# Kernel optimization log

Measured on AMD Instinct MI355X. Metric: run time of the kernel, lower is better.

The kernel has to match this reference:

```python
import jax, jax.numpy as jnp
import numpy as np

B, S, F, H = 64, 1024, 64, 128


def setup_inputs() -> dict:
    key = jax.random.key(0)
    ks = jax.random.split(key, 12)
    s = 1.0 / np.sqrt(H)
    u = lambda k, shape: jax.random.uniform(k, shape, jnp.float32, -s, s)
    return {
        "x": jax.random.normal(ks[0], (B, S, F), jnp.float32),
        "mu": jax.random.normal(ks[1], (B, 1, F), jnp.float32),
        "W_ih0": u(ks[2], (4 * H, F)),
        "W_hh0": u(ks[3], (4 * H, H)),
        "b_ih0": u(ks[4], (4 * H,)),
        "b_hh0": u(ks[5], (4 * H,)),
        "W_ih1": u(ks[6], (4 * H, H)),
        "W_hh1": u(ks[7], (4 * H, H)),
        "b_ih1": u(ks[8], (4 * H,)),
        "b_hh1": u(ks[9], (4 * H,)),
        "fc_w": u(ks[10], (1, H)),
        "fc_b": u(ks[11], (1,)),
    }


def _cell(x_gates, h, c, Whh, bias):
    # PyTorch LSTM cell: gates ordered i, f, g, o
    g = x_gates + h @ Whh.T + bias
    i, f, gg, o = jnp.split(g, 4, axis=-1)
    c = jax.nn.sigmoid(f) * c + jax.nn.sigmoid(i) * jnp.tanh(gg)
    h = jax.nn.sigmoid(o) * jnp.tanh(c)
    return h, c


def _lstm2(x1, x2, Wih, Whh, bih, bhh):
    # 2-step LSTM layer from zero initial state; returns per-step hidden states
    bias = bih + bhh
    n = x1.shape[0]
    hd = Whh.shape[1]
    h0 = jnp.zeros((n, hd), x1.dtype)
    h1, c1 = _cell(x1 @ Wih.T, h0, h0, Whh, bias)
    h2, _ = _cell(x2 @ Wih.T, h1, c1, Whh, bias)
    return h1, h2


def reference(x, mu, W_ih0, W_hh0, b_ih0, b_hh0, W_ih1, W_hh1, b_ih1, b_hh1, fc_w, fc_b):
    b, s, f = x.shape
    # Every timestep runs an independent 2-step LSTM [x_t, mu] from zero state,
    # so fold (batch, seq) into one big batch of B*S instances.
    x1 = x.reshape(b * s, f)                                   # step-1 inputs
    x2 = jnp.broadcast_to(mu, (b, s, f)).reshape(b * s, f)     # step-2 inputs (mu)
    h1, h2 = _lstm2(x1, x2, W_ih0, W_hh0, b_ih0, b_hh0)        # layer 0
    _, h2 = _lstm2(h1, h2, W_ih1, W_hh1, b_ih1, b_hh1)         # layer 1
    h = jax.nn.relu(h2).reshape(b, s, -1)                      # relu; dropout is identity (eval)
    out = h @ fc_w.T + fc_b                                    # [B, S, 1]
    return out
```

## Files before the change

### kernel.cpp

```cpp
#include <hip/hip_runtime.h>


typedef _Float16 half8 __attribute__((ext_vector_type(8)));
typedef _Float16 half4_t __attribute__((ext_vector_type(4)));
typedef float f32x4 __attribute__((ext_vector_type(4)));

#define L2E  1.4426950408889634f
#define L2E2 2.8853900817779268f

#define WP_WIH0 0
#define WP_WHH0 32768
#define WP_WIH1 98304
#define WP_WHH1 163840
#define WS_BIAS0 458752
#define WS_BIAS1 (458752 + 2048)
#define WS_MUG2  (458752 + 4096)

__global__ void prep_kernel(const float* __restrict__ Wih0,
                            const float* __restrict__ Whh0,
                            const float* __restrict__ Wih1,
                            const float* __restrict__ Whh1,
                            const float* __restrict__ bih0,
                            const float* __restrict__ bhh0,
                            const float* __restrict__ bih1,
                            const float* __restrict__ bhh1,
                            const float* __restrict__ mu,
                            _Float16* __restrict__ Wp,
                            float* __restrict__ bias0f,
                            float* __restrict__ bias1f,
                            float* __restrict__ mu_g2)
{
    int blk = blockIdx.x;
    if (blk >= 113) {
        int o = (blk - 113) * 256 + threadIdx.x;
        int b = o >> 9;
        int n = o & 511;
        float s = bih0[n] + bhh0[n];
        const float* m = mu + b * 64;
        const float* wrow = Wih0 + n * 64;
        #pragma unroll 8
        for (int k = 0; k < 64; ++k) s += m[k] * wrow[k];
        float scale = ((n >> 7) == 2) ? L2E2 : L2E;
        mu_g2[o] = s * scale;
        return;
    }
    if (blk == 112) {
        int i = threadIdx.x;
        float sc_hi = (i < 128) ? L2E2 : L2E;
        bias0f[i]       = (bih0[i]       + bhh0[i])       * L2E;
        bias0f[i + 256] = (bih0[i + 256] + bhh0[i + 256]) * sc_hi;
        bias1f[i]       = (bih1[i]       + bhh1[i])       * L2E;
        bias1f[i + 256] = (bih1[i + 256] + bhh1[i + 256]) * sc_hi;
        return;
    }
    int gidx = blk * 256 + threadIdx.x;
    const float* src; int KC, Kw, local;
    if (gidx < 4096)       { src = Wih0; KC = 2; Kw = 64;  local = gidx; }
    else if (gidx < 12288) { src = Whh0; KC = 4; Kw = 128; local = gidx - 4096; }
    else if (gidx < 20480) { src = Wih1; KC = 4; Kw = 128; local = gidx - 12288; }
    else                   { src = Whh1; KC = 4; Kw = 128; local = gidx - 20480; }
    int lane = local & 63;
    int tmp  = local >> 6;
    int kc   = tmp % KC;
    int nt   = tmp / KC;
    int n  = nt * 16 + (lane & 15);
    int k0 = kc * 32 + (lane >> 4) * 8;
    float scale = ((n >> 7) == 2) ? L2E2 : L2E;
    const float* s = src + n * Kw + k0;
    half8 hv;
    #pragma unroll
    for (int j = 0; j < 8; ++j) hv[j] = (_Float16)(s[j] * scale);
    *(half8*)(Wp + (size_t)gidx * 8) = hv;
}

__device__ __forceinline__ float sig2(float a) {
    return __builtin_amdgcn_rcpf(1.0f + __builtin_amdgcn_exp2f(-a));
}
__device__ __forceinline__ float sigtanh(float xs, float yt) {
    float d = __builtin_amdgcn_exp2f(-xs);
    float e = __builtin_amdgcn_exp2f(yt);
    return (e - 1.0f) * __builtin_amdgcn_rcpf((1.0f + d) * (1.0f + e));
}

__device__ __forceinline__ int swz(int row, int col) {
    return (row << 8) + (col ^ ((row & 7) << 4));
}

__device__ __forceinline__ void lds_barrier() {
    asm volatile("s_waitcnt lgkmcnt(0)" ::: "memory");
    __builtin_amdgcn_s_barrier();
    asm volatile("" ::: "memory");
}

template<bool SKIPF>
__device__ __forceinline__ void load_bq(half8 bq[4], const _Float16* __restrict__ Wq,
                                        int KC, int kc, int w, int lane)
{
    #pragma unroll
    for (int g = 0; g < 4; ++g) {
        if (SKIPF && g == 1) continue;
        bq[g] = *(const half8*)(Wq + (((g * 8 + w) * KC + kc) * 64 + lane) * 8);
    }
}

template<int SRC>
__device__ __forceinline__ void load_a(half8 a[4], const char* base, int kc, int c, int q)
{
    #pragma unroll
    for (int mt = 0; mt < 4; ++mt) {
        if (SRC == 0)
            a[mt] = *(const half8*)((const _Float16*)base + (mt * 16 + c) * 72 + kc * 32 + q * 8);
        else
            a[mt] = *(const half8*)(base + swz(mt * 16 + c, kc * 64 + q * 16));
    }
}

template<int KC, int SRC, bool PF, bool FIRST, bool SKIPF, bool NSKIPF>
__device__ __forceinline__ void gemm_pf(const _Float16* __restrict__ Wq,
                                        const char* Abase,
                                        const _Float16* __restrict__ Wnext, int KCnext,
                                        half8 bqc[4], const f32x4 bv[4],
                                        int w, int lane, f32x4 acc[4][4])
{
    const int c = lane & 15, q = lane >> 4;
    #pragma unroll
    for (int kc = 0; kc < KC; ++kc) {
        half8 bqn[4];
        if (kc + 1 < KC)  load_bq<SKIPF>(bqn, Wq, KC, kc + 1, w, lane);
        else if (PF)      load_bq<NSKIPF>(bqn, Wnext, KCnext, 0, w, lane);
        half8 a[4];
        load_a<SRC>(a, Abase, kc, c, q);
        __builtin_amdgcn_s_setprio(1);
        #pragma unroll
        for (int mt = 0; mt < 4; ++mt)
            #pragma unroll
            for (int g = 0; g < 4; ++g) {
                if (SKIPF && g == 1) continue;
                f32x4 cin = (FIRST && kc == 0) ? bv[g] : acc[mt][g];
                acc[mt][g] = __builtin_amdgcn_mfma_f32_16x16x32_f16(bqc[g], a[mt], cin, 0, 0, 0);
            }
        __builtin_amdgcn_s_setprio(0);
        if (kc + 1 < KC) {
            #pragma unroll
            for (int g = 0; g < 4; ++g)
                if (!(SKIPF && g == 1)) bqc[g] = bqn[g];
        } else if (PF) {
            #pragma unroll
            for (int g = 0; g < 4; ++g)
                if (!(NSKIPF && g == 1)) bqc[g] = bqn[g];
        }
    }
}

__global__ __launch_bounds__(512) void lstm_main(
    const float* __restrict__ x, const _Float16* __restrict__ Wp_in,
    const float* __restrict__ bias0f_in, const float* __restrict__ bias1f_in,
    const float* __restrict__ mu_g2_in, const float* __restrict__ fc_w_in,
    const float* __restrict__ fc_b_in, float* __restrict__ out)
{
    __shared__ __align__(16) char smem[49152];
    char* H1s  = smem;
    char* H2s  = smem + 16384;
    char* H11s = smem + 32768;
    _Float16* A0 = (_Float16*)(smem + 16384);

    const int t = threadIdx.x;
    const int w = t >> 6, lane = t & 63, c = lane & 15, q = lane >> 4;
    const int wg = blockIdx.x;
    const int b = wg >> 4;
    const int bq_idx = w * 4 + q;

    half8 bqc[4];
    load_bq<true>(bqc, Wp_in + WP_WIH0, 2, 0, w, lane);

    {
        const float* xp = x + (size_t)wg * 4096 + t * 8;
        float4 u0 = ((const float4*)xp)[0];
        float4 u1 = ((const float4*)xp)[1];
        half8 hv;
        hv[0] = (_Float16)u0.x; hv[1] = (_Float16)u0.y;
        hv[2] = (_Float16)u0.z; hv[3] = (_Float16)u0.w;
        hv[4] = (_Float16)u1.x; hv[5] = (_Float16)u1.y;
        hv[6] = (_Float16)u1.z; hv[7] = (_Float16)u1.w;
        *(half8*)(A0 + (t >> 3) * 72 + (t & 7) * 8) = hv;
        if (t < 64) out[(size_t)wg * 64 + t] = fc_b_in[0];
    }
    lds_barrier();

    f32x4 acc[4][4];
    float cc[4][4];

    {
        f32x4 bv[4];
        {
            const float* bias0f = bias0f_in; asm volatile("" : "+s"(bias0f));
            #pragma unroll
            for (int g = 0; g < 4; ++g)
                if (g != 1) bv[g] = ((const f32x4*)bias0f)[g * 32 + bq_idx];
        }
        gemm_pf<2, 0, true, true, true, false>(
            Wp_in + WP_WIH0, (const char*)A0,
            Wp_in + WP_WHH0, 4, bqc, bv, w, lane, acc);
    }
    #pragma unroll
    for (int mt = 0; mt < 4; ++mt) {
        half4_t hv;
        #pragma unroll
        for (int r = 0; r < 4; ++r) {
            float c1 = sigtanh(acc[mt][0][r], acc[mt][2][r]);
            cc[mt][r] = c1;
            hv[r] = (_Float16)sigtanh(acc[mt][3][r], c1 * L2E2);
        }
        *(half4_t*)(H1s + swz(mt * 16 + c, w * 32 + q * 8)) = hv;
    }
    lds_barrier();

    {
        f32x4 bv[4];
        {
            const float* mu_g2b = mu_g2_in + b * 512; asm volatile("" : "+s"(mu_g2b));
            #pragma unroll
            for (int g = 0; g < 4; ++g)
                bv[g] = ((const f32x4*)mu_g2b)[g * 32 + bq_idx];
        }
        gemm_pf<4, 1, true, true, false, true>(
            Wp_in + WP_WHH0, H1s,
            Wp_in + WP_WIH1, 4, bqc, bv, w, lane, acc);
    }
    #pragma unroll
    for (int mt = 0; mt < 4; ++mt) {
        half4_t hv;
        #pragma unroll
        for (int r = 0; r < 4; ++r) {
            float c2 = sig2(acc[mt][1][r]) * cc[mt][r]
                     + sigtanh(acc[mt][0][r], acc[mt][2][r]);
            hv[r] = (_Float16)sigtanh(acc[mt][3][r], c2 * L2E2);
        }
        *(half4_t*)(H2s + swz(mt * 16 + c, w * 32 + q * 8)) = hv;
    }

    {
        f32x4 bv[4];
        {
            const float* bias1f = bias1f_in; asm volatile("" : "+s"(bias1f));
            #pragma unroll
            for (int g = 0; g < 4; ++g)
                if (g != 1) bv[g] = ((const f32x4*)bias1f)[g * 32 + bq_idx];
        }
        gemm_pf<4, 1, true, true, true, false>(
            Wp_in + WP_WIH1, H1s,
            Wp_in + WP_WIH1, 4, bqc, bv, w, lane, acc);
    }
    #pragma unroll
    for (int mt = 0; mt < 4; ++mt) {
        half4_t hv;
        #pragma unroll
        for (int r = 0; r < 4; ++r) {
            float c1 = sigtanh(acc[mt][0][r], acc[mt][2][r]);
            cc[mt][r] = c1;
            hv[r] = (_Float16)sigtanh(acc[mt][3][r], c1 * L2E2);
        }
        *(half4_t*)(H11s + swz(mt * 16 + c, w * 32 + q * 8)) = hv;
    }
    lds_barrier();

    {
        f32x4 bv[4];
        {
            const float* bias1f = bias1f_in; asm volatile("" : "+s"(bias1f));
            #pragma unroll
            for (int g = 0; g < 4; ++g)
                bv[g] = ((const f32x4*)bias1f)[g * 32 + bq_idx];
        }
        gemm_pf<4, 1, true, true, false, false>(
            Wp_in + WP_WIH1, H2s,
            Wp_in + WP_WHH1, 4, bqc, bv, w, lane, acc);
    }
    gemm_pf<4, 1, false, false, false, false>(
        Wp_in + WP_WHH1, H11s,
        nullptr, 0, bqc, nullptr, w, lane, acc);

    {
        const float* fc_w = fc_w_in; asm volatile("" : "+s"(fc_w));
        f32x4 fwv = ((const f32x4*)fc_w)[bq_idx];
        #pragma unroll
        for (int mt = 0; mt < 4; ++mt) {
            float v = 0.0f;
            #pragma unroll
            for (int r = 0; r < 4; ++r) {
                float c2 = sig2(acc[mt][1][r]) * cc[mt][r]
                         + sigtanh(acc[mt][0][r], acc[mt][2][r]);
                float h  = sigtanh(acc[mt][3][r], c2 * L2E2);
                v = fmaf(fmaxf(h, 0.0f), fwv[r], v);
            }
            v += __shfl_xor(v, 16);
            v += __shfl_xor(v, 32);
            if (lane < 16)
                atomicAdd(out + (size_t)wg * 64 + mt * 16 + lane, v);
        }
    }
}

extern "C" void kernel_launch(void* const* d_in, const int* in_sizes, int n_in,
                              void* d_out, int out_size, void* d_ws, size_t ws_size,
                              hipStream_t stream)
{
    const float* x    = (const float*)d_in[0];
    const float* mu   = (const float*)d_in[1];
    const float* Wih0 = (const float*)d_in[2];
    const float* Whh0 = (const float*)d_in[3];
    const float* bih0 = (const float*)d_in[4];
    const float* bhh0 = (const float*)d_in[5];
    const float* Wih1 = (const float*)d_in[6];
    const float* Whh1 = (const float*)d_in[7];
    const float* bih1 = (const float*)d_in[8];
    const float* bhh1 = (const float*)d_in[9];
    const float* fcw  = (const float*)d_in[10];
    const float* fcb  = (const float*)d_in[11];
    float* out = (float*)d_out;

    _Float16* Wp  = (_Float16*)d_ws;
    float* bias0f = (float*)((char*)d_ws + WS_BIAS0);
    float* bias1f = (float*)((char*)d_ws + WS_BIAS1);
    float* mu_g2  = (float*)((char*)d_ws + WS_MUG2);

    hipLaunchKernelGGL(prep_kernel, dim3(241), dim3(256), 0, stream,
                       Wih0, Whh0, Wih1, Whh1, bih0, bhh0, bih1, bhh1, mu,
                       Wp, bias0f, bias1f, mu_g2);
    hipLaunchKernelGGL(lstm_main, dim3(1024), dim3(512), 0, stream,
                       x, Wp, bias0f, bias1f, mu_g2, fcw, fcb, out);
}
```

Baseline: 132.4 us.

## Double-buffer weight fragment loads with inline-asm global loads and explicit vmcnt waits

Replaces the single-register weight prefetch with two ping-pong register buffers filled by inline-asm global_load_dwordx4 using immediate offsets and a scalar base. Explicit s_waitcnt vmcnt(4) waits let two k-chunks of weights stay in flight, and bias vectors for the next stage are issued early instead of reloaded just before each GEMM. The goal is to hide global-load latency behind MFMA work across stage boundaries. In exchange it takes on fragile manual vmcnt accounting, since the waits must match the order in which loads were issued, and more register pressure.

```diff
diff --git a/kernel.cpp b/kernel.cpp
--- a/kernel.cpp
+++ b/kernel.cpp
@@ -92,64 +92,87 @@
     asm volatile("" ::: "memory");
 }
 
-template<bool SKIPF>
-__device__ __forceinline__ void load_bq(half8 bq[4], const _Float16* __restrict__ Wq,
-                                        int KC, int kc, int w, int lane)
+template<int OFF>
+__device__ __forceinline__ void gload(half8 &d, unsigned vo, const _Float16* sbase) {
+    asm volatile("global_load_dwordx4 %0, %1, %2 offset:%c3"
+                 : "=v"(d) : "v"(vo), "s"(sbase), "n"(OFF));
+}
+template<int OFF>
+__device__ __forceinline__ void gloadf(f32x4 &d, unsigned vo, const float* sbase) {
+    asm volatile("global_load_dwordx4 %0, %1, %2 offset:%c3"
+                 : "=v"(d) : "v"(vo), "s"(sbase), "n"(OFF));
+}
+#define WAIT4(s) \
+    asm volatile("s_waitcnt vmcnt(4)" : "+v"((s)[0]), "+v"((s)[1]), "+v"((s)[2]), "+v"((s)[3]))
+#define WAIT4B(s, b) \
+    asm volatile("s_waitcnt vmcnt(4)" : "+v"((s)[0]), "+v"((s)[1]), "+v"((s)[2]), "+v"((s)[3]), \
+                                        "+v"((b)[0]), "+v"((b)[1]), "+v"((b)[2]), "+v"((b)[3]))
+#define WAIT0(s) \
+    asm volatile("s_waitcnt vmcnt(0)" : "+v"((s)[0]), "+v"((s)[1]), "+v"((s)[2]), "+v"((s)[3]))
+
+template<int OFF>
+__device__ __forceinline__ void issue4(half8 s[4], const unsigned vo[4],
+                                       const _Float16* base) {
+    gload<OFF>(s[0], vo[0], base);
+    gload<OFF>(s[1], vo[1], base);
+    gload<OFF>(s[2], vo[2], base);
+    gload<OFF>(s[3], vo[3], base);
+}
+__device__ __forceinline__ void issue_bias(f32x4 bv[4], unsigned vof, const float* base) {
+    gloadf<0>   (bv[0], vof, base);
+    gloadf<512> (bv[1], vof, base);
+    gloadf<1024>(bv[2], vof, base);
+    gloadf<1536>(bv[3], vof, base);
+}
+
+__device__ __forceinline__ void load_a0(half8 a[4], const _Float16* A0,
+                                        int kc, int c, int q) {
+    #pragma unroll
+    for (int mt = 0; mt < 4; ++mt)
+        a[mt] = *(const half8*)(A0 + (mt * 16 + c) * 72 + kc * 32 + q * 8);
+}
+__device__ __forceinline__ void load_aH(half8 a[4], const char* Hb,
+                                        int kc, int c, int q) {
+    #pragma unroll
+    for (int mt = 0; mt < 4; ++mt)
+        a[mt] = *(const half8*)(Hb + swz(mt * 16 + c, kc * 64 + q * 16));
+}
+
+template<bool SKIPF, bool CIN_BV>
+__device__ __forceinline__ void mm(const half8 s[4], const half8 a[4],
+                                   const f32x4 bv[4], f32x4 acc[4][4]) {
+    __builtin_amdgcn_s_setprio(1);
+    #pragma unroll
+    for (int mt = 0; mt < 4; ++mt)
+        #pragma unroll
+        for (int g = 0; g < 4; ++g) {
+            if (SKIPF && g == 1) continue;
+            f32x4 cin = CIN_BV ? bv[g] : acc[mt][g];
+            acc[mt][g] = __builtin_amdgcn_mfma_f32_16x16x32_f16(s[g], a[mt], cin, 0, 0, 0);
+        }
+    __builtin_amdgcn_s_setprio(0);
+}
+
+template<bool SKIPF, bool PF, bool FIRST, bool BN>
+__device__ __forceinline__ void stage4(const char* Ab, const unsigned vo[4],
+                                       const _Float16* wq, const _Float16* wqn,
+                                       const float* bnext, unsigned vof,
+                                       half8 sA[4], half8 sB[4], f32x4 bv[4],
+                                       int c, int q, f32x4 acc[4][4])
 {
-    #pragma unroll
-    for (int g = 0; g < 4; ++g) {
-        if (SKIPF && g == 1) continue;
-        bq[g] = *(const half8*)(Wq + (((g * 8 + w) * KC + kc) * 64 + lane) * 8);
-    }
-}
-
-template<int SRC>
-__device__ __forceinline__ void load_a(half8 a[4], const char* base, int kc, int c, int q)
-{
-    #pragma unroll
-    for (int mt = 0; mt < 4; ++mt) {
-        if (SRC == 0)
-            a[mt] = *(const half8*)((const _Float16*)base + (mt * 16 + c) * 72 + kc * 32 + q * 8);
-        else
-            a[mt] = *(const half8*)(base + swz(mt * 16 + c, kc * 64 + q * 16));
-    }
-}
-
-template<int KC, int SRC, bool PF, bool FIRST, bool SKIPF, bool NSKIPF>
-__device__ __forceinline__ void gemm_pf(const _Float16* __restrict__ Wq,
-                                        const char* Abase,
-                                        const _Float16* __restrict__ Wnext, int KCnext,
-                                        half8 bqc[4], const f32x4 bv[4],
-                                        int w, int lane, f32x4 acc[4][4])
-{
-    const int c = lane & 15, q = lane >> 4;
-    #pragma unroll
-    for (int kc = 0; kc < KC; ++kc) {
-        half8 bqn[4];
-        if (kc + 1 < KC)  load_bq<SKIPF>(bqn, Wq, KC, kc + 1, w, lane);
-        else if (PF)      load_bq<NSKIPF>(bqn, Wnext, KCnext, 0, w, lane);
-        half8 a[4];
-        load_a<SRC>(a, Abase, kc, c, q);
-        __builtin_amdgcn_s_setprio(1);
-        #pragma unroll
-        for (int mt = 0; mt < 4; ++mt)
-            #pragma unroll
-            for (int g = 0; g < 4; ++g) {
-                if (SKIPF && g == 1) continue;
-                f32x4 cin = (FIRST && kc == 0) ? bv[g] : acc[mt][g];
-                acc[mt][g] = __builtin_amdgcn_mfma_f32_16x16x32_f16(bqc[g], a[mt], cin, 0, 0, 0);
-            }
-        __builtin_amdgcn_s_setprio(0);
-        if (kc + 1 < KC) {
-            #pragma unroll
-            for (int g = 0; g < 4; ++g)
-                if (!(SKIPF && g == 1)) bqc[g] = bqn[g];
-        } else if (PF) {
-            #pragma unroll
-            for (int g = 0; g < 4; ++g)
-                if (!(NSKIPF && g == 1)) bqc[g] = bqn[g];
-        }
-    }
+    if constexpr (FIRST) { WAIT4B(sA, bv); } else { WAIT4(sA); }
+    { half8 a[4]; load_aH(a, Ab, 0, c, q); mm<SKIPF, FIRST>(sA, a, bv, acc); }
+    issue4<2048>(sA, vo, wq);
+    WAIT4(sB);
+    { half8 a[4]; load_aH(a, Ab, 1, c, q); mm<SKIPF, false>(sB, a, bv, acc); }
+    issue4<3072>(sB, vo, wq);
+    WAIT4(sA);
+    { half8 a[4]; load_aH(a, Ab, 2, c, q); mm<SKIPF, false>(sA, a, bv, acc); }
+    if constexpr (BN) issue_bias(bv, vof, bnext);
+    if constexpr (PF) issue4<0>(sA, vo, wqn);
+    if constexpr (PF) { WAIT4(sB); } else { WAIT0(sB); }
+    { half8 a[4]; load_aH(a, Ab, 3, c, q); mm<SKIPF, false>(sB, a, bv, acc); }
+    if constexpr (PF) issue4<1024>(sB, vo, wqn);
 }
 
 __global__ __launch_bounds__(512) void lstm_main(
@@ -170,8 +193,25 @@
     const int b = wg >> 4;
     const int bq_idx = w * 4 + q;
 
-    half8 bqc[4];
-    load_bq<true>(bqc, Wp_in + WP_WIH0, 2, 0, w, lane);
+    const _Float16* wS1  = Wp_in + WP_WIH0;
+    const _Float16* wS2  = Wp_in + WP_WHH0;
+    const _Float16* wS3  = Wp_in + WP_WIH1;
+    const _Float16* wS4b = Wp_in + WP_WHH1;
+    const float* mu_g2b  = mu_g2_in + b * 512;
+
+    unsigned voA[4], voB[4];
+    #pragma unroll
+    for (int g = 0; g < 4; ++g) {
+        voA[g] = (unsigned)(((g * 8 + w) * 1024 + lane * 8) * 2);
+        voB[g] = (unsigned)(((g * 8 + w) * 2048 + lane * 8) * 2);
+    }
+    unsigned vof = (unsigned)(bq_idx * 16);
+
+    half8 sA[4], sB[4];
+    f32x4 bv[4];
+    issue4<0>(sA, voA, wS1);
+    issue_bias(bv, vof, bias0f_in);
+    issue4<1024>(sB, voA, wS1);
 
     {
         const float* xp = x + (size_t)wg * 4096 + t * 8;
@@ -190,18 +230,13 @@
     f32x4 acc[4][4];
     float cc[4][4];
 
-    {
-        f32x4 bv[4];
-        {
-            const float* bias0f = bias0f_in; asm volatile("" : "+s"(bias0f));
-            #pragma unroll
-            for (int g = 0; g < 4; ++g)
-                if (g != 1) bv[g] = ((const f32x4*)bias0f)[g * 32 + bq_idx];
-        }
-        gemm_pf<2, 0, true, true, true, false>(
-            Wp_in + WP_WIH0, (const char*)A0,
-            Wp_in + WP_WHH0, 4, bqc, bv, w, lane, acc);
-    }
+    WAIT4B(sA, bv);
+    { half8 a[4]; load_a0(a, A0, 0, c, q); mm<true, true>(sA, a, bv, acc); }
+    issue_bias(bv, vof, mu_g2b);
+    issue4<0>(sA, voB, wS2);
+    WAIT4(sB);
+    { half8 a[4]; load_a0(a, A0, 1, c, q); mm<true, false>(sB, a, bv, acc); }
+    issue4<1024>(sB, voB, wS2);
     #pragma unroll
     for (int mt = 0; mt < 4; ++mt) {
         half4_t hv;
@@ -215,18 +250,8 @@
     }
     lds_barrier();
 
-    {
-        f32x4 bv[4];
-        {
-            const float* mu_g2b = mu_g2_in + b * 512; asm volatile("" : "+s"(mu_g2b));
-            #pragma unroll
-            for (int g = 0; g < 4; ++g)
-                bv[g] = ((const f32x4*)mu_g2b)[g * 32 + bq_idx];
-        }
-        gemm_pf<4, 1, true, true, false, true>(
-            Wp_in + WP_WHH0, H1s,
-            Wp_in + WP_WIH1, 4, bqc, bv, w, lane, acc);
-    }
+    stage4<false, true, true, true>(H1s, voB, wS2, wS3, bias1f_in, vof,
+                                    sA, sB, bv, c, q, acc);
     #pragma unroll
     for (int mt = 0; mt < 4; ++mt) {
         half4_t hv;
@@ -239,18 +264,8 @@
         *(half4_t*)(H2s + swz(mt * 16 + c, w * 32 + q * 8)) = hv;
     }
 
-    {
-        f32x4 bv[4];
-        {
-            const float* bias1f = bias1f_in; asm volatile("" : "+s"(bias1f));
-            #pragma unroll
-            for (int g = 0; g < 4; ++g)
-                if (g != 1) bv[g] = ((const f32x4*)bias1f)[g * 32 + bq_idx];
-        }
-        gemm_pf<4, 1, true, true, true, false>(
-            Wp_in + WP_WIH1, H1s,
-            Wp_in + WP_WIH1, 4, bqc, bv, w, lane, acc);
-    }
+    stage4<true, true, true, true>(H1s, voB, wS3, wS3, bias1f_in, vof,
+                                   sA, sB, bv, c, q, acc);
     #pragma unroll
     for (int mt = 0; mt < 4; ++mt) {
         half4_t hv;
@@ -264,21 +279,10 @@
     }
     lds_barrier();
 
-    {
-        f32x4 bv[4];
-        {
-            const float* bias1f = bias1f_in; asm volatile("" : "+s"(bias1f));
-            #pragma unroll
-            for (int g = 0; g < 4; ++g)
-                bv[g] = ((const f32x4*)bias1f)[g * 32 + bq_idx];
-        }
-        gemm_pf<4, 1, true, true, false, false>(
-            Wp_in + WP_WIH1, H2s,
-            Wp_in + WP_WHH1, 4, bqc, bv, w, lane, acc);
-    }
-    gemm_pf<4, 1, false, false, false, false>(
-        Wp_in + WP_WHH1, H11s,
-        nullptr, 0, bqc, nullptr, w, lane, acc);
+    stage4<false, true, true, false>(H2s, voB, wS3, wS4b, nullptr, vof,
+                                     sA, sB, bv, c, q, acc);
+    stage4<false, false, false, false>(H11s, voB, wS4b, nullptr, nullptr, vof,
+                                       sA, sB, bv, c, q, acc);
 
     {
         const float* fc_w = fc_w_in; asm volatile("" : "+s"(fc_w));
```

Result: slower. 135.9 us (+2.6%).
